# Optimization experiments

Measured on AMD Instinct MI355X. Metric: run time of the kernel, lower is better.

The kernel has to match this reference:

```python
import jax, jax.numpy as jnp
import numpy as np

B, T, Fd, C, D = 16, 256, 128, 32, 32
K_RATIO = 0.5
EPS = 1e-5


def setup_inputs() -> dict:
    key = jax.random.key(0)
    ks = jax.random.split(key, 40)
    n = lambda i, shape, s=0.05: jax.random.normal(ks[i], shape, jnp.float32) * s
    inp = {"x": jax.random.normal(ks[0], (B, T, Fd, C), jnp.float32)}
    inp.update(c1w=n(1, (C, C)), c1b=n(2, (C,)), bng=1.0 + n(3, (C,)), bnb=n(4, (C,)),
               bnm=n(5, (C,)), bnv=jax.random.uniform(ks[6], (C,)) + 0.5,
               c2w=n(7, (1, C)), c2b=n(8, (1,)))
    def gat_params(i0, pre):
        return {pre + "apw": n(i0, (D, C)), pre + "apb": n(i0 + 1, (D,)),
                pre + "aw": n(i0 + 2, (D,)), pre + "pww": n(i0 + 3, (D, C)),
                pre + "pwb": n(i0 + 4, (D,)), pre + "pow": n(i0 + 5, (D, C)),
                pre + "pob": n(i0 + 6, (D,)), pre + "g": 1.0 + n(i0 + 7, (D,)),
                pre + "be": n(i0 + 8, (D,)), pre + "m": n(i0 + 9, (D,)),
                pre + "v": jax.random.uniform(ks[i0 + 10], (D,)) + 0.5}
    inp.update(gat_params(9, "fc_"))
    inp.update(gat_params(20, "tc_"))
    inp.update(pfw=n(31, (1, D)), pfb=n(32, (1,)), ptw=n(33, (1, D)), ptb=n(34, (1,)),
               w1=n(35, (D, D)), w2=n(36, (D, D)), fcw=n(37, (2, 2 * D)), fcb=n(38, (2,)))
    return inp


def _gat(h, apw, apb, aw, pww, pwb, poww, pob, g, be, mu, var):
    # h: (B, N, C). Dense pairwise multiplication -> (B, N, N, C)
    p = h[:, :, None, :] * h[:, None, :, :]
    e = jnp.tanh(jnp.einsum('bijc,dc->bijd', p, apw) + apb)      # (B,N,N,D)
    att = jax.nn.softmax(jnp.einsum('bijd,d->bij', e, aw), axis=2)  # softmax over dim=-2 (temp=1)
    out = jnp.einsum('bij,bjc->bic', att, h) @ pww.T + pwb + h @ poww.T + pob
    out = (out - mu) / jnp.sqrt(var + EPS) * g + be               # BatchNorm1d (eval)
    return jax.nn.selu(out)


def _pool(h, pw, pb, ratio):
    s = jax.nn.sigmoid(h @ pw.T + pb)                # (B,N,1)
    kn = max(int(h.shape[1] * ratio), 1)
    _, idx = jax.lax.top_k(s[..., 0], kn)            # (B,kn), descending scores
    return jnp.take_along_axis(h * s, idx[..., None], axis=1)


def reference(x, c1w, c1b, bng, bnb, bnm, bnv, c2w, c2b,
              fc_apw, fc_apb, fc_aw, fc_pww, fc_pwb, fc_pow, fc_pob, fc_g, fc_be, fc_m, fc_v,
              tc_apw, tc_apb, tc_aw, tc_pww, tc_pwb, tc_pow, tc_pob, tc_g, tc_be, tc_m, tc_v,
              pfw, pfb, ptw, ptb, w1, w2, fcw, fcb):
    # conv1 (1x1), SELU, BatchNorm2d (eval), conv2 (1x1 -> 1 channel)
    xp = jnp.einsum('oc,btfc->botf', c1w, x) + c1b[None, :, None, None]
    xp = jax.nn.selu(xp)
    xp = (xp - bnm[None, :, None, None]) / jnp.sqrt(bnv + EPS)[None, :, None, None] \
         * bng[None, :, None, None] + bnb[None, :, None, None]
    m = jnp.einsum('c,bctf->btf', c2w[0], xp) + c2b[0]           # (B,T,F)
    M0 = jax.nn.softmax(m, axis=1)
    FCatt = jnp.einsum('btf,btfc->bfc', M0, x)                   # sum over T
    TCatt = jnp.einsum('btf,btfc->btc', M0, x)                   # sum over F
    FC_gat = _gat(FCatt, fc_apw, fc_apb, fc_aw, fc_pww, fc_pwb, fc_pow, fc_pob, fc_g, fc_be, fc_m, fc_v)
    TC_gat = _gat(TCatt, tc_apw, tc_apb, tc_aw, tc_pww, tc_pwb, tc_pow, tc_pob, tc_g, tc_be, tc_m, tc_v)
    xF = _pool(FC_gat, pfw, pfb, K_RATIO)                        # (B, F/2, D)
    xT = _pool(TC_gat, ptw, ptb, K_RATIO)                        # (B, T/2, D)
    M1 = jax.nn.softmax((xF @ w1.T) @ xT.transpose(0, 2, 1), axis=-1)
    M2 = jax.nn.softmax((xT @ w2.T) @ xF.transpose(0, 2, 1), axis=-1)
    xF_fused = xF + M1 @ xT
    xT_fused = xT + M2 @ xF
    node = jnp.concatenate([xF_fused.max(axis=1), xT_fused.max(axis=1)], axis=-1)
    return node @ fcw.T + fcb
```

## Files before the change

### kernel.cpp

```cpp
#include <hip/hip_runtime.h>
#include <hip/hip_bf16.h>

#define Bn 16
#define Tn 256
#define Fn 128
#define Cn 32
#define Dn 32
#define EPSf 1e-5f
#define SELU_L 1.0507009873554805f
#define SELU_A 1.6732632423543772f

typedef unsigned short u16;
typedef unsigned int u32;

struct Ptrs { const void* p[39]; };

#define P_C1W 0
#define P_C1B 1024
#define P_MW  1056
#define P_MK  1088
#define P_FC  1089
#define P_TCG (1089+3264)
#define G_APW 0
#define G_APB 1024
#define G_AW  1056
#define G_PWW 1088
#define G_PWB 2112
#define G_POW 2144
#define G_POB 3168
#define G_GS  3200
#define G_GB  3232
#define GAT_SZ 3264
#define P_PFW (P_TCG+GAT_SZ)
#define P_PFB (P_PFW+32)
#define P_PTW (P_PFB+1)
#define P_PTB (P_PTW+32)
#define P_W1  (P_PTB+1)
#define P_W2  (P_W1+1024)
#define P_FCW (P_W2+1024)
#define P_FCB (P_FCW+128)
#define P_FLAG 10000

#define WS_M     10240
#define WS_FCATT (WS_M+524288)
#define WS_TCATT (WS_FCATT+65536)
#define WS_FCGAT (WS_TCATT+131072)
#define WS_TCGAT (WS_FCGAT+65536)
#define WS_XF    (WS_TCGAT+131072)
#define WS_XT    (WS_XF+32768)
#define WS_XFF   (WS_XT+65536)
#define WS_XTF   (WS_XFF+32768)

__device__ __forceinline__ float bf2f(u16 u) {
    union { u32 i; float f; } v; v.i = ((u32)u) << 16; return v.f;
}
__device__ __forceinline__ u16 f2bf(float f) {
    union { float f; u32 u; } v; v.f = f;
    u32 r = (v.u + 0x7fffu + ((v.u >> 16) & 1u)) >> 16;
    return (u16)r;
}
__device__ __forceinline__ void up2(u32 u, float* o) {
    union { u32 i; float f; } a, b;
    a.i = u << 16; b.i = u & 0xffff0000u;
    o[0] = a.f; o[1] = b.f;
}
__device__ __forceinline__ float tanh_fast(float x) {
    float e = __expf(2.f * x);
    return 1.f - 2.f / (e + 1.f);
}
__device__ __forceinline__ float ldp(const void* p, int i, int isb) {
    return isb ? bf2f(((const u16*)p)[i]) : ((const float*)p)[i];
}

__global__ __launch_bounds__(256) void k0_setup(Ptrs in, float* __restrict__ P) {
    __shared__ int sflag;
    int tid = threadIdx.x;
    int blk = blockIdx.x;
    if (tid < 64) {
        const u16* xu = (const u16*)in.p[0];
        int bad = 0;
        #pragma unroll
        for (int q = 0; q < 4; q++) {
            float f = bf2f(xu[tid * 4 + q]);
            float a = fabsf(f);
            if (!(a < 64.f) && !(a == 0.f)) bad++;
        }
        #pragma unroll
        for (int off = 32; off >= 1; off >>= 1) bad += __shfl_xor(bad, off, 64);
        if (tid == 0) sflag = (bad <= 8) ? 1 : 0;
    }
    __syncthreads();
    const int isb = sflag;

    if (blk == 0) {
        if (tid == 0) P[P_FLAG] = (float)isb;
        for (int i = tid; i < 1024; i += 256) P[P_C1W + i] = ldp(in.p[1], i, isb);
        if (tid < 32) {
            float A = ldp(in.p[3], tid, isb) * rsqrtf(ldp(in.p[6], tid, isb) + EPSf);
            float w = ldp(in.p[7], tid, isb);
            P[P_C1B + tid] = ldp(in.p[2], tid, isb);
            P[P_MW + tid] = w * A * SELU_L;
            float Bc = ldp(in.p[4], tid, isb) - ldp(in.p[5], tid, isb) * A;
            float term = w * Bc;
            #pragma unroll
            for (int off = 16; off >= 1; off >>= 1) term += __shfl_xor(term, off, 64);
            if (tid == 0) P[P_MK] = term + ldp(in.p[8], 0, isb);
        }
        if (tid >= 64 && tid < 96) {
            int t = tid - 64;
            P[P_PFW + t] = ldp(in.p[31], t, isb);
            P[P_PTW + t] = ldp(in.p[33], t, isb);
        }
        if (tid == 96) { P[P_PFB] = ldp(in.p[32], 0, isb); P[P_PTB] = ldp(in.p[34], 0, isb); }
        if (tid == 97) P[P_FCB]     = ldp(in.p[38], 0, isb);
        if (tid == 98) P[P_FCB + 1] = ldp(in.p[38], 1, isb);
        if (tid >= 128) P[P_FCW + (tid - 128)] = ldp(in.p[37], tid - 128, isb);
    } else if (blk <= 2) {
        int g = blk - 1;
        int ib = g ? 20 : 9;
        float* G = P + (g ? P_TCG : P_FC);
        for (int i = tid; i < 1024; i += 256) {
            G[G_APW + i] = ldp(in.p[ib + 0], i, isb);
            G[G_PWW + i] = ldp(in.p[ib + 3], i, isb);
            G[G_POW + i] = ldp(in.p[ib + 5], i, isb);
        }
        if (tid < 32) {
            G[G_APB + tid] = ldp(in.p[ib + 1], tid, isb);
            G[G_AW  + tid] = ldp(in.p[ib + 2], tid, isb);
            G[G_PWB + tid] = ldp(in.p[ib + 4], tid, isb);
            G[G_POB + tid] = ldp(in.p[ib + 6], tid, isb);
            float gs = ldp(in.p[ib + 7], tid, isb) * rsqrtf(ldp(in.p[ib + 10], tid, isb) + EPSf);
            G[G_GS + tid] = gs;
            G[G_GB + tid] = ldp(in.p[ib + 8], tid, isb) - ldp(in.p[ib + 9], tid, isb) * gs;
        }
    } else {
        for (int i = tid; i < 1024; i += 256) {
            P[P_W1 + i] = ldp(in.p[35], i, isb);
            P[P_W2 + i] = ldp(in.p[36], i, isb);
        }
    }
}

__global__ __launch_bounds__(256) void k1_conv_m(const void* __restrict__ xin,
                                                 const float* __restrict__ P,
                                                 float* __restrict__ M) {
    int idx = blockIdx.x * 256 + threadIdx.x;
    const int isb = __builtin_amdgcn_readfirstlane((int)P[P_FLAG]);
    float xv[32];
    if (isb) {
        const uint4* xp4 = reinterpret_cast<const uint4*>((const u16*)xin + (size_t)idx * 32);
        uint4 q0 = xp4[0], q1 = xp4[1], q2 = xp4[2], q3 = xp4[3];
        up2(q0.x, xv + 0);  up2(q0.y, xv + 2);  up2(q0.z, xv + 4);  up2(q0.w, xv + 6);
        up2(q1.x, xv + 8);  up2(q1.y, xv + 10); up2(q1.z, xv + 12); up2(q1.w, xv + 14);
        up2(q2.x, xv + 16); up2(q2.y, xv + 18); up2(q2.z, xv + 20); up2(q2.w, xv + 22);
        up2(q3.x, xv + 24); up2(q3.y, xv + 26); up2(q3.z, xv + 28); up2(q3.w, xv + 30);
    } else {
        const float4* xf4 = reinterpret_cast<const float4*>((const float*)xin + (size_t)idx * 32);
        #pragma unroll
        for (int q = 0; q < 8; q++) {
            float4 v = xf4[q];
            xv[q * 4 + 0] = v.x; xv[q * 4 + 1] = v.y;
            xv[q * 4 + 2] = v.z; xv[q * 4 + 3] = v.w;
        }
    }
    float acc = P[P_MK];
    #pragma unroll
    for (int o = 0; o < 32; o++) {
        float z = P[P_C1B + o];
        #pragma unroll
        for (int c = 0; c < 32; c++) z = fmaf(P[P_C1W + o * 32 + c], xv[c], z);
        float br = (z > 0.f) ? z : SELU_A * (__expf(z) - 1.f);
        acc = fmaf(P[P_MW + o], br, acc);
    }
    M[idx] = acc;
}

__global__ __launch_bounds__(256) void k2_softmax(float* __restrict__ M,
                                                  float* __restrict__ FCzero) {
    __shared__ float r[256];
    int b = blockIdx.x >> 3, fg = blockIdx.x & 7;
    int tid = threadIdx.x;
    int fl = tid & 15, ts = tid >> 4;
    float* col = M + (size_t)b * (Tn * Fn) + fg * 16 + fl;
    float v[16];
    float mx = -1e30f;
    #pragma unroll
    for (int k = 0; k < 16; k++) { v[k] = col[(ts * 16 + k) * Fn]; mx = fmaxf(mx, v[k]); }
    r[tid] = mx; __syncthreads();
    for (int s = 128; s >= 16; s >>= 1) { if (tid < s) r[tid] = fmaxf(r[tid], r[tid + s]); __syncthreads(); }
    mx = r[fl];
    __syncthreads();
    float sm = 0.f;
    #pragma unroll
    for (int k = 0; k < 16; k++) { v[k] = __expf(v[k] - mx); sm += v[k]; }
    r[tid] = sm; __syncthreads();
    for (int s = 128; s >= 16; s >>= 1) { if (tid < s) r[tid] += r[tid + s]; __syncthreads(); }
    float inv = 1.f / r[fl];
    #pragma unroll
    for (int k = 0; k < 16; k++) col[(ts * 16 + k) * Fn] = v[k] * inv;
    int gid = blockIdx.x * 256 + tid;
    for (int i = gid; i < Bn * Fn * Cn; i += 128 * 256) FCzero[i] = 0.f;
}

__global__ __launch_bounds__(256) void k3n(const void* __restrict__ xin,
                                           const float* __restrict__ M,
                                           const float* __restrict__ Pflag,
                                           float* __restrict__ FCatt,
                                           float* __restrict__ TCatt) {
    __shared__ float part[4][8][32];
    int bi = blockIdx.x;
    int b = bi >> 5, tg = bi & 31;
    int tid = threadIdx.x;
    int w = tid >> 6, lane = tid & 63;
    const int isb = __builtin_amdgcn_readfirstlane((int)Pflag[P_FLAG]);
    float fa0[8], fa1[8];
    #pragma unroll
    for (int k = 0; k < 8; k++) { fa0[k] = 0.f; fa1[k] = 0.f; }
    int fbase = tid >> 4;
    for (int tt = 0; tt < 8; tt++) {
        int t = tg * 8 + tt;
        const float* Mrow = M + (size_t)b * (Tn * Fn) + (size_t)t * Fn;
        size_t rowoff = ((size_t)b * Tn + t) * (Fn * Cn);
        float ts0 = 0.f, ts1 = 0.f;
        #pragma unroll
        for (int k = 0; k < 8; k++) {
            float x0, x1;
            if (isb) {
                u32 u = *(const u32*)((const u16*)xin + rowoff + tid * 2 + 512 * k);
                float tmp[2]; up2(u, tmp); x0 = tmp[0]; x1 = tmp[1];
            } else {
                float2 v2 = *(const float2*)((const float*)xin + rowoff + tid * 2 + 512 * k);
                x0 = v2.x; x1 = v2.y;
            }
            float m = Mrow[fbase + 16 * k];
            x0 *= m; x1 *= m;
            fa0[k] += x0; fa1[k] += x1;
            ts0 += x0; ts1 += x1;
        }
        ts0 += __shfl_xor(ts0, 16, 64); ts0 += __shfl_xor(ts0, 32, 64);
        ts1 += __shfl_xor(ts1, 16, 64); ts1 += __shfl_xor(ts1, 32, 64);
        if (lane < 16) {
            part[w][tt][lane * 2]     = ts0;
            part[w][tt][lane * 2 + 1] = ts1;
        }
    }
    __syncthreads();
    {
        int tt = tid >> 5, c = tid & 31;
        float s = part[0][tt][c] + part[1][tt][c] + part[2][tt][c] + part[3][tt][c];
        TCatt[((size_t)b * Tn + tg * 8 + tt) * Cn + c] = s;
    }
    #pragma unroll
    for (int k = 0; k < 8; k++) {
        atomicAdd(&FCatt[(size_t)b * 4096 + tid * 2 + 512 * k],     fa0[k]);
        atomicAdd(&FCatt[(size_t)b * 4096 + tid * 2 + 512 * k + 1], fa1[k]);
    }
}

__global__ __launch_bounds__(256) void k4a_scores(const float* __restrict__ P,
                                                  const float* __restrict__ FCatt,
                                                  const float* __restrict__ TCatt,
                                                  u16* __restrict__ SFC,
                                                  u16* __restrict__ STC) {
    __shared__ float li[16 * 33], lj[16 * 33];
    int bi = blockIdx.x;
    int N, nt, b, pr; const float* h; u16* S; const float* G;
    if (bi < 16 * 36) { b = bi / 36; pr = bi % 36; N = 128; nt = 8;
        h = FCatt + (size_t)b * 4096; S = SFC + (size_t)b * 16384; G = P + P_FC; }
    else { bi -= 16 * 36; b = bi / 136; pr = bi % 136; N = 256; nt = 16;
        h = TCatt + (size_t)b * 8192; S = STC + (size_t)b * 65536; G = P + P_TCG; }
    int ti = 0, rem = pr;
    while (rem >= nt - ti) { rem -= nt - ti; ti++; }
    int tj = ti + rem;
    int tid = threadIdx.x;
    for (int e = tid; e < 512; e += 256) {
        int rr = e >> 5, c = e & 31;
        li[rr * 33 + c] = h[(ti * 16 + rr) * 32 + c];
        lj[rr * 33 + c] = h[(tj * 16 + rr) * 32 + c];
    }
    __syncthreads();
    int il = tid >> 4, jl = tid & 15;
    float p[32];
    #pragma unroll
    for (int c = 0; c < 32; c++) p[c] = li[il * 33 + c] * lj[jl * 33 + c];
    float score = 0.f;
    #pragma unroll
    for (int d = 0; d < 32; d++) {
        float z = G[G_APB + d];
        #pragma unroll
        for (int c = 0; c < 32; c++) z = fmaf(G[G_APW + d * 32 + c], p[c], z);
        score = fmaf(G[G_AW + d], tanh_fast(z), score);
    }
    int i = ti * 16 + il, j = tj * 16 + jl;
    u16 sb = f2bf(score);
    S[(size_t)i * N + j] = sb;
    if (ti != tj) S[(size_t)j * N + i] = sb;
}

__global__ __launch_bounds__(256) void k4b_soft(const float* __restrict__ P,
                                                const float* __restrict__ FCatt,
                                                const float* __restrict__ TCatt,
                                                const u16* __restrict__ SFC,
                                                const u16* __restrict__ STC,
                                                float* __restrict__ FCgat,
                                                float* __restrict__ TCgat) {
    __shared__ float hs[256 * 32];
    __shared__ float scb[4][256];
    int bi = blockIdx.x;
    int N, b, rowbase; const float* h; float* out; const float* G; const u16* S;
    if (bi < 128) {
        N = 128; b = bi >> 3; rowbase = (bi & 7) * 16;
        h = FCatt + (size_t)b * 4096; out = FCgat + (size_t)b * 4096; G = P + P_FC;
        S = SFC + (size_t)b * 16384;
    } else {
        int t = bi - 128;
        N = 256; b = t >> 4; rowbase = (t & 15) * 16;
        h = TCatt + (size_t)b * 8192; out = TCgat + (size_t)b * 8192; G = P + P_TCG;
        S = STC + (size_t)b * 65536;
    }
    int tid = threadIdx.x;
    int w = tid >> 6, lane = tid & 63;
    const float4* h4 = reinterpret_cast<const float4*>(h);
    float4* hs4 = reinterpret_cast<float4*>(hs);
    for (int el = tid; el < N * 8; el += 256) hs4[el] = h4[el];
    __syncthreads();

    int c = lane & 31;
    int nq = N >> 6;
    for (int r = 0; r < 4; r++) {
        int row = rowbase + w + 4 * r;
        const u16* Srow = S + (size_t)row * N;
        float v[4];
        float mx = -1e30f;
        for (int q = 0; q < nq; q++) { v[q] = bf2f(Srow[lane + 64 * q]); mx = fmaxf(mx, v[q]); }
        #pragma unroll
        for (int off = 32; off >= 1; off >>= 1) mx = fmaxf(mx, __shfl_xor(mx, off, 64));
        float sum = 0.f;
        for (int q = 0; q < nq; q++) {
            float e = __expf(v[q] - mx);
            scb[w][lane + 64 * q] = e;
            sum += e;
        }
        #pragma unroll
        for (int off = 32; off >= 1; off >>= 1) sum += __shfl_xor(sum, off, 64);
        float inv = 1.f / sum;
        asm volatile("s_waitcnt lgkmcnt(0)" ::: "memory");
        int half = lane >> 5;
        float acc = 0.f;
        for (int j = half; j < N; j += 2) acc = fmaf(scb[w][j], hs[j * 32 + c], acc);
        acc += __shfl_xor(acc, 32, 64);
        acc *= inv;
        int d = c;
        float z = G[G_PWB + d] + G[G_POB + d];
        #pragma unroll
        for (int c2 = 0; c2 < 32; c2++)
            z = fmaf(G[G_PWW + d * 32 + c2], __shfl(acc, c2, 64),
                fmaf(G[G_POW + d * 32 + c2], hs[row * 32 + c2], z));
        z = z * G[G_GS + d] + G[G_GB + d];
        z = SELU_L * ((z > 0.f) ? z : SELU_A * (__expf(z) - 1.f));
        if (lane < 32) out[(size_t)row * 32 + d] = z;
    }
}

__global__ __launch_bounds__(256) void k5_pool(const float* __restrict__ P,
                                               const float* __restrict__ FCgat,
                                               const float* __restrict__ TCgat,
                                               float* __restrict__ XF,
                                               float* __restrict__ XT) {
    __shared__ float s[256];
    int bi = blockIdx.x;
    int N, kn, b, pboff; const float* g; float* xp; const float* pw;
    if (bi < 16) { b = bi; N = 128; kn = 64;
        g = FCgat + (size_t)b * 4096; xp = XF + (size_t)b * 2048; pw = P + P_PFW; pboff = P_PFB; }
    else { b = bi - 16; N = 256; kn = 128;
        g = TCgat + (size_t)b * 8192; xp = XT + (size_t)b * 4096; pw = P + P_PTW; pboff = P_PTB; }
    int tid = threadIdx.x;
    float sv = 0.f;
    if (tid < N) {
        float z = P[pboff];
        #pragma unroll
        for (int d = 0; d < 32; d++) z = fmaf(pw[d], g[(size_t)tid * 32 + d], z);
        sv = 1.f / (1.f + __expf(-z));
        s[tid] = sv;
    }
    __syncthreads();
    if (tid < N) {
        int rank = 0;
        for (int l = 0; l < N; l++) {
            float sl = s[l];
            rank += (sl > sv) || (sl == sv && l < tid);
        }
        if (rank < kn) {
            #pragma unroll
            for (int d = 0; d < 32; d++) xp[(size_t)rank * 32 + d] = g[(size_t)tid * 32 + d] * sv;
        }
    }
}

__global__ __launch_bounds__(256) void k6_fuse(const float* __restrict__ P,
                                               const float* __restrict__ XF,
                                               const float* __restrict__ XT,
                                               float* __restrict__ XFF,
                                               float* __restrict__ XTF) {
    int wid = blockIdx.x * 4 + (threadIdx.x >> 6);
    int lane = threadIdx.x & 63;
    if (wid < 1024) {
        int b = wid >> 6, i = wid & 63;
        const float* xf  = XF + ((size_t)b * 64 + i) * 32;
        const float* xtb = XT + (size_t)b * 4096;
        const float* w1 = P + P_W1;
        int d = lane & 31;
        float y = 0.f;
        #pragma unroll
        for (int c = 0; c < 32; c++) y = fmaf(w1[d * 32 + c], xf[c], y);
        float xtr0[32], xtr1[32];
        #pragma unroll
        for (int c = 0; c < 32; c++) {
            xtr0[c] = xtb[(size_t)lane * 32 + c];
            xtr1[c] = xtb[(size_t)(lane + 64) * 32 + c];
        }
        float s0 = 0.f, s1 = 0.f;
        #pragma unroll
        for (int c = 0; c < 32; c++) {
            float yc = __shfl(y, c, 64);
            s0 = fmaf(yc, xtr0[c], s0);
            s1 = fmaf(yc, xtr1[c], s1);
        }
        float mx = fmaxf(s0, s1);
        #pragma unroll
        for (int off = 1; off < 64; off <<= 1) mx = fmaxf(mx, __shfl_xor(mx, off, 64));
        float e0 = __expf(s0 - mx), e1 = __expf(s1 - mx);
        float sm = e0 + e1;
        #pragma unroll
        for (int off = 1; off < 64; off <<= 1) sm += __shfl_xor(sm, off, 64);
        float inv = 1.f / sm;
        float a0 = e0 * inv, a1 = e1 * inv;
        float v[32];
        #pragma unroll
        for (int c = 0; c < 32; c++) v[c] = a0 * xtr0[c] + a1 * xtr1[c];
        #pragma unroll
        for (int off = 1; off < 64; off <<= 1) {
            #pragma unroll
            for (int c = 0; c < 32; c++) v[c] += __shfl_xor(v[c], off, 64);
        }
        if (lane == 0) {
            float* o = XFF + ((size_t)b * 64 + i) * 32;
            #pragma unroll
            for (int c = 0; c < 32; c++) o[c] = xf[c] + v[c];
        }
    } else {
        int r = wid - 1024;
        int b = r >> 7, i = r & 127;
        const float* xt  = XT + ((size_t)b * 128 + i) * 32;
        const float* xfb = XF + (size_t)b * 2048;
        const float* w2 = P + P_W2;
        int d = lane & 31;
        float y = 0.f;
        #pragma unroll
        for (int c = 0; c < 32; c++) y = fmaf(w2[d * 32 + c], xt[c], y);
        float xfr[32];
        #pragma unroll
        for (int c = 0; c < 32; c++) xfr[c] = xfb[(size_t)lane * 32 + c];
        float sc0 = 0.f;
        #pragma unroll
        for (int c = 0; c < 32; c++) sc0 = fmaf(__shfl(y, c, 64), xfr[c], sc0);
        float mx = sc0;
        #pragma unroll
        for (int off = 1; off < 64; off <<= 1) mx = fmaxf(mx, __shfl_xor(mx, off, 64));
        float e = __expf(sc0 - mx);
        float sm = e;
        #pragma unroll
        for (int off = 1; off < 64; off <<= 1) sm += __shfl_xor(sm, off, 64);
        float a = e / sm;
        float v[32];
        #pragma unroll
        for (int c = 0; c < 32; c++) v[c] = a * xfr[c];
        #pragma unroll
        for (int off = 1; off < 64; off <<= 1) {
            #pragma unroll
            for (int c = 0; c < 32; c++) v[c] += __shfl_xor(v[c], off, 64);
        }
        if (lane == 0) {
            float* o = XTF + ((size_t)b * 128 + i) * 32;
            #pragma unroll
            for (int c = 0; c < 32; c++) o[c] = xt[c] + v[c];
        }
    }
}

__global__ __launch_bounds__(64) void k7_out(const float* __restrict__ P,
                                             const float* __restrict__ XFF,
                                             const float* __restrict__ XTF,
                                             void* __restrict__ outp) {
    __shared__ float node[64];
    int b = blockIdx.x, tid = threadIdx.x;
    if (tid < 32) {
        float m = -1e30f;
        for (int r = 0; r < 64; r++) m = fmaxf(m, XFF[((size_t)b * 64 + r) * 32 + tid]);
        node[tid] = m;
    } else {
        int c = tid - 32;
        float m = -1e30f;
        for (int r = 0; r < 128; r++) m = fmaxf(m, XTF[((size_t)b * 128 + r) * 32 + c]);
        node[tid] = m;
    }
    __syncthreads();
    if (tid < 2) {
        float z = P[P_FCB + tid];
        #pragma unroll
        for (int k = 0; k < 64; k++) z = fmaf(P[P_FCW + tid * 64 + k], node[k], z);
        int isb = (int)P[P_FLAG];
        if (isb) ((u16*)outp)[b * 2 + tid] = f2bf(z);
        else     ((float*)outp)[b * 2 + tid] = z;
    }
}

extern "C" void kernel_launch(void* const* d_in, const int* in_sizes, int n_in,
                              void* d_out, int out_size, void* d_ws, size_t ws_size,
                              hipStream_t stream) {
    (void)in_sizes; (void)n_in; (void)out_size; (void)ws_size;
    float* W = (float*)d_ws;
    Ptrs ptrs;
    for (int i = 0; i < 39; i++) ptrs.p[i] = d_in[i];
    const void* x = d_in[0];
    float* P = W;
    u16* STC = (u16*)(W + WS_M);
    u16* SFC = (u16*)(W + WS_XF);

    k0_setup<<<4, 256, 0, stream>>>(ptrs, P);
    k1_conv_m<<<2048, 256, 0, stream>>>(x, P, W + WS_M);
    k2_softmax<<<128, 256, 0, stream>>>(W + WS_M, W + WS_FCATT);
    k3n<<<512, 256, 0, stream>>>(x, W + WS_M, P, W + WS_FCATT, W + WS_TCATT);
    k4a_scores<<<16 * 36 + 16 * 136, 256, 0, stream>>>(P, W + WS_FCATT, W + WS_TCATT, SFC, STC);
    k4b_soft<<<384, 256, 0, stream>>>(P, W + WS_FCATT, W + WS_TCATT, SFC, STC,
                                      W + WS_FCGAT, W + WS_TCGAT);
    k5_pool<<<32, 256, 0, stream>>>(P, W + WS_FCGAT, W + WS_TCGAT, W + WS_XF, W + WS_XT);
    k6_fuse<<<768, 256, 0, stream>>>(P, W + WS_XF, W + WS_XT, W + WS_XFF, W + WS_XTF);
    k7_out<<<16, 64, 0, stream>>>(P, W + WS_XFF, W + WS_XTF, d_out);
}
```

Measured before the change: 337.1 us.

## Use bf16 MFMA for the pointwise conv and the GAT pairwise score projection

The 1x1 conv in k1 (bf16 input path) and the pairwise attention projection in k4a are rewritten to use 16x16x32 bf16 MFMA instructions in place of scalar FMA loops. Each wave processes 16-row tiles and reduces the weighted SELU/tanh outputs across lanes with shuffles. k4a now computes the full score matrix per row block with h staged in shared memory, dropping the symmetric-tile scheme, and both kernels use fewer, larger blocks. This removes most of the scalar FMA work. In exchange, weights and the pairwise products are rounded to bf16 before accumulation, and k4a computes the symmetric half of the score matrix twice.

```diff
diff --git a/kernel.cpp b/kernel.cpp
--- a/kernel.cpp
+++ b/kernel.cpp
@@ -12,6 +12,8 @@
 
 typedef unsigned short u16;
 typedef unsigned int u32;
+typedef __attribute__((ext_vector_type(8))) short bf16x8;
+typedef __attribute__((ext_vector_type(4))) float f32x4;
 
 struct Ptrs { const void* p[39]; };
 
@@ -144,35 +146,69 @@
 __global__ __launch_bounds__(256) void k1_conv_m(const void* __restrict__ xin,
                                                  const float* __restrict__ P,
                                                  float* __restrict__ M) {
-    int idx = blockIdx.x * 256 + threadIdx.x;
     const int isb = __builtin_amdgcn_readfirstlane((int)P[P_FLAG]);
-    float xv[32];
+    int tid = threadIdx.x;
     if (isb) {
-        const uint4* xp4 = reinterpret_cast<const uint4*>((const u16*)xin + (size_t)idx * 32);
-        uint4 q0 = xp4[0], q1 = xp4[1], q2 = xp4[2], q3 = xp4[3];
-        up2(q0.x, xv + 0);  up2(q0.y, xv + 2);  up2(q0.z, xv + 4);  up2(q0.w, xv + 6);
-        up2(q1.x, xv + 8);  up2(q1.y, xv + 10); up2(q1.z, xv + 12); up2(q1.w, xv + 14);
-        up2(q2.x, xv + 16); up2(q2.y, xv + 18); up2(q2.z, xv + 20); up2(q2.w, xv + 22);
-        up2(q3.x, xv + 24); up2(q3.y, xv + 26); up2(q3.z, xv + 28); up2(q3.w, xv + 30);
+        int w = tid >> 6, lane = tid & 63;
+        int n = lane & 15, g = lane >> 4, kc = g * 8;
+        bf16x8 b0, b1;
+        #pragma unroll
+        for (int e = 0; e < 8; e++) {
+            b0[e] = (short)f2bf(P[P_C1W + n * 32 + kc + e]);
+            b1[e] = (short)f2bf(P[P_C1W + (n + 16) * 32 + kc + e]);
+        }
+        float cb0 = P[P_C1B + n], cb1 = P[P_C1B + n + 16];
+        float mw0 = P[P_MW + n],  mw1 = P[P_MW + n + 16];
+        float mk = P[P_MK];
+        int rowblk = blockIdx.x * 512 + w * 128;
+        for (int s = 0; s < 8; s++) {
+            int r0 = rowblk + s * 16;
+            const u16* xp = (const u16*)xin + (size_t)r0 * 32;
+            bf16x8 a = *(const bf16x8*)(xp + (size_t)(lane & 15) * 32 + kc);
+            f32x4 c0 = {0.f, 0.f, 0.f, 0.f}, c1 = {0.f, 0.f, 0.f, 0.f};
+            c0 = __builtin_amdgcn_mfma_f32_16x16x32_bf16(a, b0, c0, 0, 0, 0);
+            c1 = __builtin_amdgcn_mfma_f32_16x16x32_bf16(a, b1, c1, 0, 0, 0);
+            float acc[4];
+            #pragma unroll
+            for (int r = 0; r < 4; r++) {
+                float z0 = c0[r] + cb0, z1 = c1[r] + cb1;
+                float s0 = (z0 > 0.f) ? z0 : SELU_A * (__expf(z0) - 1.f);
+                float s1 = (z1 > 0.f) ? z1 : SELU_A * (__expf(z1) - 1.f);
+                acc[r] = fmaf(mw0, s0, mw1 * s1);
+            }
+            #pragma unroll
+            for (int off = 1; off < 16; off <<= 1) {
+                #pragma unroll
+                for (int r = 0; r < 4; r++) acc[r] += __shfl_xor(acc[r], off, 64);
+            }
+            if (n == 0) {
+                float4 o4 = make_float4(acc[0] + mk, acc[1] + mk, acc[2] + mk, acc[3] + mk);
+                *(float4*)(M + (size_t)r0 + g * 4) = o4;
+            }
+        }
     } else {
-        const float4* xf4 = reinterpret_cast<const float4*>((const float*)xin + (size_t)idx * 32);
-        #pragma unroll
-        for (int q = 0; q < 8; q++) {
-            float4 v = xf4[q];
-            xv[q * 4 + 0] = v.x; xv[q * 4 + 1] = v.y;
-            xv[q * 4 + 2] = v.z; xv[q * 4 + 3] = v.w;
-        }
-    }
-    float acc = P[P_MK];
-    #pragma unroll
-    for (int o = 0; o < 32; o++) {
-        float z = P[P_C1B + o];
-        #pragma unroll
-        for (int c = 0; c < 32; c++) z = fmaf(P[P_C1W + o * 32 + c], xv[c], z);
-        float br = (z > 0.f) ? z : SELU_A * (__expf(z) - 1.f);
-        acc = fmaf(P[P_MW + o], br, acc);
-    }
-    M[idx] = acc;
+        for (int rr = 0; rr < 2; rr++) {
+            int idx = blockIdx.x * 512 + rr * 256 + tid;
+            float xv[32];
+            const float4* xf4 = reinterpret_cast<const float4*>((const float*)xin + (size_t)idx * 32);
+            #pragma unroll
+            for (int q = 0; q < 8; q++) {
+                float4 v = xf4[q];
+                xv[q * 4 + 0] = v.x; xv[q * 4 + 1] = v.y;
+                xv[q * 4 + 2] = v.z; xv[q * 4 + 3] = v.w;
+            }
+            float acc = P[P_MK];
+            #pragma unroll
+            for (int o = 0; o < 32; o++) {
+                float z = P[P_C1B + o];
+                #pragma unroll
+                for (int c = 0; c < 32; c++) z = fmaf(P[P_C1W + o * 32 + c], xv[c], z);
+                float br = (z > 0.f) ? z : SELU_A * (__expf(z) - 1.f);
+                acc = fmaf(P[P_MW + o], br, acc);
+            }
+            M[idx] = acc;
+        }
+    }
 }
 
 __global__ __launch_bounds__(256) void k2_softmax(float* __restrict__ M,
@@ -262,39 +298,64 @@
                                                   const float* __restrict__ TCatt,
                                                   u16* __restrict__ SFC,
                                                   u16* __restrict__ STC) {
-    __shared__ float li[16 * 33], lj[16 * 33];
+    __shared__ float hs[256 * 36];
     int bi = blockIdx.x;
-    int N, nt, b, pr; const float* h; u16* S; const float* G;
-    if (bi < 16 * 36) { b = bi / 36; pr = bi % 36; N = 128; nt = 8;
+    int N, b, ib0, jslog; const float* h; u16* S; const float* G;
+    if (bi < 128) { N = 128; b = bi >> 3; ib0 = (bi & 7) * 16; jslog = 3;
         h = FCatt + (size_t)b * 4096; S = SFC + (size_t)b * 16384; G = P + P_FC; }
-    else { bi -= 16 * 36; b = bi / 136; pr = bi % 136; N = 256; nt = 16;
+    else { int t = bi - 128; N = 256; b = t >> 4; ib0 = (t & 15) * 16; jslog = 4;
         h = TCatt + (size_t)b * 8192; S = STC + (size_t)b * 65536; G = P + P_TCG; }
-    int ti = 0, rem = pr;
-    while (rem >= nt - ti) { rem -= nt - ti; ti++; }
-    int tj = ti + rem;
     int tid = threadIdx.x;
-    for (int e = tid; e < 512; e += 256) {
-        int rr = e >> 5, c = e & 31;
-        li[rr * 33 + c] = h[(ti * 16 + rr) * 32 + c];
-        lj[rr * 33 + c] = h[(tj * 16 + rr) * 32 + c];
+    int w = tid >> 6, lane = tid & 63;
+    int n = lane & 15, g = lane >> 4, kc = g * 8;
+
+    bf16x8 b0, b1;
+    #pragma unroll
+    for (int e = 0; e < 8; e++) {
+        b0[e] = (short)f2bf(G[G_APW + n * 32 + kc + e]);
+        b1[e] = (short)f2bf(G[G_APW + (n + 16) * 32 + kc + e]);
+    }
+    float aw0 = G[G_AW + n],  aw1 = G[G_AW + n + 16];
+    float ab0 = G[G_APB + n], ab1 = G[G_APB + n + 16];
+
+    const float4* h4 = reinterpret_cast<const float4*>(h);
+    for (int el = tid; el < N * 8; el += 256) {
+        float4 v = h4[el];
+        int row = el >> 3, c = (el & 7) * 4;
+        *(float4*)&hs[row * 36 + c] = v;
     }
     __syncthreads();
-    int il = tid >> 4, jl = tid & 15;
-    float p[32];
-    #pragma unroll
-    for (int c = 0; c < 32; c++) p[c] = li[il * 33 + c] * lj[jl * 33 + c];
-    float score = 0.f;
-    #pragma unroll
-    for (int d = 0; d < 32; d++) {
-        float z = G[G_APB + d];
-        #pragma unroll
-        for (int c = 0; c < 32; c++) z = fmaf(G[G_APW + d * 32 + c], p[c], z);
-        score = fmaf(G[G_AW + d], tanh_fast(z), score);
-    }
-    int i = ti * 16 + il, j = tj * 16 + jl;
-    u16 sb = f2bf(score);
-    S[(size_t)i * N + j] = sb;
-    if (ti != tj) S[(size_t)j * N + i] = sb;
+
+    int steps = (16 << jslog) >> 2;
+    int jmask = (1 << jslog) - 1;
+    for (int s = 0; s < steps; s++) {
+        int st = s * 4 + w;
+        int i = ib0 + (st >> jslog);
+        int j0 = (st & jmask) << 4;
+        const float* hi = &hs[i * 36 + kc];
+        const float* hj = &hs[(j0 + n) * 36 + kc];
+        bf16x8 a;
+        #pragma unroll
+        for (int e = 0; e < 8; e++) a[e] = (short)f2bf(hi[e] * hj[e]);
+        f32x4 c0 = {0.f, 0.f, 0.f, 0.f}, c1 = {0.f, 0.f, 0.f, 0.f};
+        c0 = __builtin_amdgcn_mfma_f32_16x16x32_bf16(a, b0, c0, 0, 0, 0);
+        c1 = __builtin_amdgcn_mfma_f32_16x16x32_bf16(a, b1, c1, 0, 0, 0);
+        float sc[4];
+        #pragma unroll
+        for (int r = 0; r < 4; r++)
+            sc[r] = fmaf(aw0, tanh_fast(c0[r] + ab0), aw1 * tanh_fast(c1[r] + ab1));
+        #pragma unroll
+        for (int off = 1; off < 16; off <<= 1) {
+            #pragma unroll
+            for (int r = 0; r < 4; r++) sc[r] += __shfl_xor(sc[r], off, 64);
+        }
+        if (n == 0) {
+            union { u16 q[4]; uint2 v; } pk;
+            #pragma unroll
+            for (int r = 0; r < 4; r++) pk.q[r] = f2bf(sc[r]);
+            *(uint2*)(S + (size_t)i * N + j0 + g * 4) = pk.v;
+        }
+    }
 }
 
 __global__ __launch_bounds__(256) void k4b_soft(const float* __restrict__ P,
@@ -528,10 +589,10 @@
     u16* SFC = (u16*)(W + WS_XF);
 
     k0_setup<<<4, 256, 0, stream>>>(ptrs, P);
-    k1_conv_m<<<2048, 256, 0, stream>>>(x, P, W + WS_M);
+    k1_conv_m<<<1024, 256, 0, stream>>>(x, P, W + WS_M);
     k2_softmax<<<128, 256, 0, stream>>>(W + WS_M, W + WS_FCATT);
     k3n<<<512, 256, 0, stream>>>(x, W + WS_M, P, W + WS_FCATT, W + WS_TCATT);
-    k4a_scores<<<16 * 36 + 16 * 136, 256, 0, stream>>>(P, W + WS_FCATT, W + WS_TCATT, SFC, STC);
+    k4a_scores<<<384, 256, 0, stream>>>(P, W + WS_FCATT, W + WS_TCATT, SFC, STC);
     k4b_soft<<<384, 256, 0, stream>>>(P, W + WS_FCATT, W + WS_TCATT, SFC, STC,
                                       W + WS_FCGAT, W + WS_TCGAT);
     k5_pool<<<32, 256, 0, stream>>>(P, W + WS_FCGAT, W + WS_TCGAT, W + WS_XF, W + WS_XT);
```

After: 392.9 us. +16.6%, slower.
